# Kernel optimization log

Hardware: AMD Instinct MI355X
Metric: run time of the kernel (lower is better)

Reference implementation:

```python
import jax, jax.numpy as jnp
import numpy as np

NEG_INF = -1e9  # matches masked_fill value in torch code
LRELU_ALPHA = 0.2


def setup_inputs() -> dict:
    key = jax.random.key(0)
    k1, k2, k3, k4 = jax.random.split(key, 4)
    B, N, F_IN, H, DK = 4, 2048, 128, 4, 32
    x = jax.random.normal(k1, (B, N, F_IN), dtype=jnp.float32)
    adj = jax.random.randint(k2, (B, N, N), 0, 2, dtype=jnp.int32)
    # xavier-ish scaled params
    W = jax.random.normal(k3, (H, F_IN, DK), dtype=jnp.float32) * (1.0 / np.sqrt(F_IN))
    a = jax.random.normal(k4, (H, 2 * DK, 1), dtype=jnp.float32) * (1.0 / np.sqrt(2 * DK))
    return {"x": x, "adj": adj, "W": W, "a": a}


def reference(x, adj, W, a):
    B, N, _ = x.shape
    H, _, DK = W.shape
    # h: (B, H, N, DK)
    h = jnp.einsum('bni,hio->bhno', x, W)
    # Split attention vector: e[b,h,i,j] = h_i.a_l + h_j.a_r  (avoids O(N^2 * 2d) concat)
    a_l = a[:, :DK, 0]   # (H, DK)
    a_r = a[:, DK:, 0]   # (H, DK)
    el = jnp.einsum('bhnd,hd->bhn', h, a_l)  # (B, H, N)
    er = jnp.einsum('bhnd,hd->bhn', h, a_r)  # (B, H, N)
    e = el[:, :, :, None] + er[:, :, None, :]          # (B, H, N, N)
    e = jax.nn.leaky_relu(e, negative_slope=LRELU_ALPHA)
    e = jnp.where(adj[:, None, :, :] == 0, NEG_INF, e)
    alpha = jax.nn.softmax(e, axis=-1)                 # dropout is identity (eval)
    h_prime = jnp.einsum('bhij,bhjd->bhid', alpha, h)  # (B, H, N, DK)
    # torch code does h_prime.view(B, N, -1) on contiguous (B,H,N,DK): raw reshape
    out = h_prime.reshape(B, N, H * DK)
    return out
```

## Files before the change

### kernel.cpp

```cpp
#include <hip/hip_runtime.h>
#include <stdint.h>

#define LOG2E 1.4426950408889634f

typedef __bf16 v8bf __attribute__((ext_vector_type(8)));
typedef float v16f __attribute__((ext_vector_type(16)));

static constexpr int B = 4, N = 2048, FIN = 128, H = 4, DK = 32;
static constexpr int IT = N / 32;
static constexpr int PACK_BLOCKS = B * N * N / 1024;
static constexpr int PREP_BLOCKS = (B * N * FIN + H * DK * FIN) / 256;

__device__ __forceinline__ float exp2_fast(float x) {
#if __has_builtin(__builtin_amdgcn_exp2f)
  return __builtin_amdgcn_exp2f(x);
#else
  float r;
  asm("v_exp_f32 %0, %1" : "=v"(r) : "v"(x));
  return r;
#endif
}

__device__ __forceinline__ unsigned int bf16_rne(float f) {
  unsigned int u = __builtin_bit_cast(unsigned int, f);
  u += 0x7FFFu + ((u >> 16) & 1u);
  return u >> 16;
}

__global__ __launch_bounds__(256) void k_prep(const int* __restrict__ adj,
                                              const float* __restrict__ x,
                                              const float* __restrict__ W,
                                              unsigned int* __restrict__ adjb,
                                              unsigned short* __restrict__ xb,
                                              unsigned short* __restrict__ wtb) {
  int bid = blockIdx.x;
  int tid = threadIdx.x;
  if (bid < PACK_BLOCKS) {
    int wid = (bid * 256 + tid) >> 6;
    int lane = tid & 63;
    const int* p = adj + (size_t)wid * 256 + lane;
    unsigned long long m0 = __ballot(p[0] != 0);
    unsigned long long m1 = __ballot(p[64] != 0);
    unsigned long long m2 = __ballot(p[128] != 0);
    unsigned long long m3 = __ballot(p[192] != 0);
    if (lane == 0) {
      uint4 v0 = {(unsigned)m0, (unsigned)(m0 >> 32), (unsigned)m1, (unsigned)(m1 >> 32)};
      uint4 v1 = {(unsigned)m2, (unsigned)(m2 >> 32), (unsigned)m3, (unsigned)(m3 >> 32)};
      uint4* dst = (uint4*)(adjb + (size_t)wid * 8);
      dst[0] = v0;
      dst[1] = v1;
    }
    return;
  }
  int idx = (bid - PACK_BLOCKS) * 256 + tid;
  constexpr int TX = B * N * FIN;
  if (idx < TX) {
    xb[idx] = (unsigned short)bf16_rne(x[idx]);
  } else {
    int j = idx - TX;
    int h = j >> 12, r = j & 4095, d = r >> 7, f = r & 127;
    wtb[j] = (unsigned short)bf16_rne(W[(h * FIN + f) * DK + d]);
  }
}

__global__ __launch_bounds__(256) void k_hproj(const unsigned short* __restrict__ xb,
                                               const unsigned short* __restrict__ wtb,
                                               const float* __restrict__ a,
                                               unsigned short* __restrict__ h_t,
                                               float* __restrict__ el,
                                               float* __restrict__ er) {
  int blk = blockIdx.x;
  int b = blk >> 6, it = blk & 63;
  int tid = threadIdx.x;
  int head = tid >> 6, lane = tid & 63;
  int lrow = lane & 31, kh = lane >> 5;
  int bh = b * H + head;
  int n = it * 32 + lrow;
  const unsigned short* xp = xb + (b * N + n) * FIN + kh * 8;
  const unsigned short* wp = wtb + (head * DK + lrow) * FIN + kh * 8;
  v16f acc = {};
#pragma unroll
  for (int s = 0; s < FIN / 16; ++s) {
    v8bf av = __builtin_bit_cast(v8bf, *(const int4*)(wp + s * 16));
    v8bf bv = __builtin_bit_cast(v8bf, *(const int4*)(xp + s * 16));
    acc = __builtin_amdgcn_mfma_f32_32x32x16_bf16(av, bv, acc, 0, 0, 0);
  }
  float pel = 0.f, per = 0.f;
#pragma unroll
  for (int r = 0; r < 16; ++r) {
    int d = (r & 3) + 8 * (r >> 2) + 4 * kh;
    float hv = acc[r];
    h_t[(bh * DK + d) * N + n] = (unsigned short)bf16_rne(hv);
    pel = fmaf(hv, a[head * 2 * DK + d], pel);
    per = fmaf(hv, a[head * 2 * DK + DK + d], per);
  }
  pel += __shfl_xor(pel, 32);
  per += __shfl_xor(per, 32);
  if (kh == 0) {
    el[bh * N + n] = pel * LOG2E;
    er[bh * N + n] = per * LOG2E;
  }
}

__global__ __launch_bounds__(1024, 8) void k_attn(const unsigned int* __restrict__ adjb,
                                                  const unsigned short* __restrict__ h_t,
                                                  const float* __restrict__ el,
                                                  const float* __restrict__ er,
                                                  float* __restrict__ pnum,
                                                  float* __restrict__ pden) {
  __shared__ __align__(16) float part4[4][H][1024];
  __shared__ float lsh4[4][H][32];
  int blk = blockIdx.x;
  int bit = blk >> 1, jh = blk & 1;
  int b = bit >> 6, it = bit & 63;
  int tid = threadIdx.x;
  int wave = tid >> 6;
  int head = wave & 3, jq = wave >> 2;
  int lane = tid & 63, lrow = lane & 31, kh = lane >> 5;
  int ig = it * 32 + lrow, bh = b * H + head;

  {
    int hh = tid >> 8, jl = (tid & 255) * 4;
    *(float4*)&part4[0][hh][jl] = *(const float4*)&er[(b * H + hh) * N + jh * 1024 + jl];
  }

  float eli = el[bh * N + ig];
  int j0 = jh * 1024 + jq * 256 + kh * 8;
  const unsigned short* hp = h_t + (size_t)(bh * DK + lrow) * N + j0;
  int jql = jq * 256 + kh * 8;

  const uint4* abp = (const uint4*)(adjb + (size_t)(b * N + ig) * 64 + jh * 32 + jq * 8);
  uint4 ab0 = abp[0], ab1 = abp[1];
  unsigned adw[8] = {ab0.x, ab0.y, ab0.z, ab0.w, ab1.x, ab1.y, ab1.z, ab1.w};
  int shkh = kh * 8;

  int4 hreg0 = *(const int4*)hp;
  int4 hreg1 = *(const int4*)(hp + 16);

  __syncthreads();

  v16f acc = {};
  float lsum = 0.f;
  float4 Ea = *(const float4*)&part4[0][head][jql];
  float4 Eb = *(const float4*)&part4[0][head][jql + 4];
#pragma unroll
  for (int s = 0; s < 16; ++s) {
    int4 hb = (s & 1) ? hreg1 : hreg0;
    if (s + 2 < 16) {
      int4 nv = *(const int4*)(hp + (s + 2) * 16);
      if (s & 1) hreg1 = nv; else hreg0 = nv;
    }
    float4 ea = Ea, eb = Eb;
    if (s + 1 < 16) {
      Ea = *(const float4*)&part4[0][head][jql + (s + 1) * 16];
      Eb = *(const float4*)&part4[0][head][jql + (s + 1) * 16 + 4];
    }
    unsigned mb = (adw[s >> 1] >> (((s & 1) * 16) + shkh)) & 0xFFu;
    float ev[8] = {ea.x, ea.y, ea.z, ea.w, eb.x, eb.y, eb.z, eb.w};
    unsigned ub[8];
#pragma unroll
    for (int k = 0; k < 8; ++k) {
      float tt = eli + ev[k];
      tt = fmaxf(tt, 0.2f * tt);
      float pv = exp2_fast(tt);
      unsigned u = __builtin_bit_cast(unsigned, pv) & 0xFFFF0000u;
      u = (mb & (1u << k)) ? u : 0u;
      ub[k] = u;
      lsum += __builtin_bit_cast(float, u);
    }
    unsigned u0 = __builtin_amdgcn_perm(ub[1], ub[0], 0x07060302u);
    unsigned u1 = __builtin_amdgcn_perm(ub[3], ub[2], 0x07060302u);
    unsigned u2 = __builtin_amdgcn_perm(ub[5], ub[4], 0x07060302u);
    unsigned u3 = __builtin_amdgcn_perm(ub[7], ub[6], 0x07060302u);
    uint4 au = {u0, u1, u2, u3};
    v8bf av = __builtin_bit_cast(v8bf, au);
    v8bf hv = __builtin_bit_cast(v8bf, hb);
    acc = __builtin_amdgcn_mfma_f32_32x32x16_bf16(av, hv, acc, 0, 0, 0);
  }

  lsum += __shfl_xor(lsum, 32);
  if (lane < 32) lsh4[jq][head][lane] = lsum;

  __syncthreads();

#pragma unroll
  for (int r = 0; r < 16; ++r) {
    int rowl = (r & 3) + 8 * (r >> 2) + 4 * kh;
    part4[jq][head][rowl * 32 + lrow] = acc[r];
  }
  __syncthreads();

  int e = tid * 4;
  int rh = e >> 10, rr = e & 1023;
  float4 q0 = *(const float4*)&part4[0][rh][rr];
  float4 q1 = *(const float4*)&part4[1][rh][rr];
  float4 q2 = *(const float4*)&part4[2][rh][rr];
  float4 q3 = *(const float4*)&part4[3][rh][rr];
  float4 s4;
  s4.x = (q0.x + q1.x) + (q2.x + q3.x);
  s4.y = (q0.y + q1.y) + (q2.y + q3.y);
  s4.z = (q0.z + q1.z) + (q2.z + q3.z);
  s4.w = (q0.w + q1.w) + (q2.w + q3.w);
  *(float4*)&pnum[(size_t)blk * 4096 + e] = s4;
  if (tid < 128) {
    float d = (lsh4[0][tid >> 5][tid & 31] + lsh4[1][tid >> 5][tid & 31]) +
              (lsh4[2][tid >> 5][tid & 31] + lsh4[3][tid >> 5][tid & 31]);
    pden[blk * 128 + tid] = d;
  }
}

__global__ __launch_bounds__(1024) void k_final(const float* __restrict__ pnum,
                                                const float* __restrict__ pden,
                                                float* __restrict__ out) {
  int bit = blockIdx.x;
  int b = bit >> 6, it = bit & 63;
  int tid = threadIdx.x;
  int e = tid * 4;
  int rh = e >> 10, ri = (e >> 5) & 31, rd = e & 31;
  size_t p0 = (size_t)(bit * 2) * 4096 + e;
  float4 n0 = *(const float4*)&pnum[p0];
  float4 n1 = *(const float4*)&pnum[p0 + 4096];
  float d = pden[bit * 2 * 128 + rh * 32 + ri] + pden[(bit * 2 + 1) * 128 + rh * 32 + ri];
  float inv = 1.0f / d;
  float4 o;
  o.x = (n0.x + n1.x) * inv;
  o.y = (n0.y + n1.y) * inv;
  o.z = (n0.z + n1.z) * inv;
  o.w = (n0.w + n1.w) * inv;
  *(float4*)&out[(size_t)((b * H + rh) * N + it * 32 + ri) * DK + rd] = o;
}

extern "C" void kernel_launch(void* const* d_in, const int* in_sizes, int n_in,
                              void* d_out, int out_size, void* d_ws, size_t ws_size,
                              hipStream_t stream) {
  const float* x = (const float*)d_in[0];
  const int* adj = (const int*)d_in[1];
  const float* W = (const float*)d_in[2];
  const float* a = (const float*)d_in[3];
  float* out = (float*)d_out;
  char* ws = (char*)d_ws;

  unsigned short* h_t = (unsigned short*)(ws);
  float* el = (float*)(ws + 0x200000);
  float* er = (float*)(ws + 0x220000);
  unsigned short* wtb = (unsigned short*)(ws + 0x240000);
  unsigned int* adjb = (unsigned int*)(ws + 0x250000);
  unsigned short* xb = (unsigned short*)(ws + 0x450000);
  float* pnum = (float*)(ws + 0x650000);
  float* pden = (float*)(ws + 0xE50000);

  hipLaunchKernelGGL(k_prep, dim3(PACK_BLOCKS + PREP_BLOCKS), dim3(256), 0, stream,
                     adj, x, W, adjb, xb, wtb);
  hipLaunchKernelGGL(k_hproj, dim3(B * IT), dim3(256), 0, stream, xb, wtb, a, h_t, el, er);
  hipLaunchKernelGGL(k_attn, dim3(B * IT * 2), dim3(1024), 0, stream, adjb, h_t, el, er, pnum, pden);
  hipLaunchKernelGGL(k_final, dim3(B * IT), dim3(1024), 0, stream, pnum, pden, out);
}
```

Baseline: 128.9 us.

## Store h in MFMA fragment layout for coalesced attention B-operand loads

The projection kernel now runs a second transposed MFMA, takes the output in accumulator layout, and writes h as pre-packed per-lane bf16 MFMA fragments instead of scattered 2-byte transposed stores. The attention kernel then reads each B operand as contiguous 16-byte per-lane loads with a 512-element stride. The j indexing, adjacency mask bits and e-vector offsets are remapped to match the accumulator's interleaved k ordering. The cost is one extra MFMA chain in the projection and more intricate index bookkeeping that must match exactly.

```diff
diff --git a/kernel.cpp b/kernel.cpp
--- a/kernel.cpp
+++ b/kernel.cpp
@@ -66,7 +66,7 @@
 __global__ __launch_bounds__(256) void k_hproj(const unsigned short* __restrict__ xb,
                                                const unsigned short* __restrict__ wtb,
                                                const float* __restrict__ a,
-                                               unsigned short* __restrict__ h_t,
+                                               unsigned short* __restrict__ h_frag,
                                                float* __restrict__ el,
                                                float* __restrict__ er) {
   int blk = blockIdx.x;
@@ -79,18 +79,30 @@
   const unsigned short* xp = xb + (b * N + n) * FIN + kh * 8;
   const unsigned short* wp = wtb + (head * DK + lrow) * FIN + kh * 8;
   v16f acc = {};
+  v16f accd = {};
 #pragma unroll
   for (int s = 0; s < FIN / 16; ++s) {
     v8bf av = __builtin_bit_cast(v8bf, *(const int4*)(wp + s * 16));
     v8bf bv = __builtin_bit_cast(v8bf, *(const int4*)(xp + s * 16));
     acc = __builtin_amdgcn_mfma_f32_32x32x16_bf16(av, bv, acc, 0, 0, 0);
+    accd = __builtin_amdgcn_mfma_f32_32x32x16_bf16(bv, av, accd, 0, 0, 0);
+  }
+  {
+    unsigned w[8];
+#pragma unroll
+    for (int i = 0; i < 8; ++i)
+      w[i] = bf16_rne(accd[2 * i]) | (bf16_rne(accd[2 * i + 1]) << 16);
+    unsigned short* fp = h_frag + (((size_t)bh * 128 + it * 2) * 64 + lane) * 8;
+    int4 v0 = {(int)w[0], (int)w[1], (int)w[2], (int)w[3]};
+    int4 v1 = {(int)w[4], (int)w[5], (int)w[6], (int)w[7]};
+    *(int4*)fp = v0;
+    *(int4*)(fp + 512) = v1;
   }
   float pel = 0.f, per = 0.f;
 #pragma unroll
   for (int r = 0; r < 16; ++r) {
     int d = (r & 3) + 8 * (r >> 2) + 4 * kh;
     float hv = acc[r];
-    h_t[(bh * DK + d) * N + n] = (unsigned short)bf16_rne(hv);
     pel = fmaf(hv, a[head * 2 * DK + d], pel);
     per = fmaf(hv, a[head * 2 * DK + DK + d], per);
   }
@@ -103,7 +115,7 @@
 }
 
 __global__ __launch_bounds__(1024, 8) void k_attn(const unsigned int* __restrict__ adjb,
-                                                  const unsigned short* __restrict__ h_t,
+                                                  const unsigned short* __restrict__ h_frag,
                                                   const float* __restrict__ el,
                                                   const float* __restrict__ er,
                                                   float* __restrict__ pnum,
@@ -125,38 +137,39 @@
   }
 
   float eli = el[bh * N + ig];
-  int j0 = jh * 1024 + jq * 256 + kh * 8;
-  const unsigned short* hp = h_t + (size_t)(bh * DK + lrow) * N + j0;
-  int jql = jq * 256 + kh * 8;
+  const unsigned short* hp =
+      h_frag + (((size_t)bh * 128 + jh * 64 + jq * 16) * 64 + lane) * 8;
+  int jql = jq * 256 + 4 * kh;
 
   const uint4* abp = (const uint4*)(adjb + (size_t)(b * N + ig) * 64 + jh * 32 + jq * 8);
   uint4 ab0 = abp[0], ab1 = abp[1];
   unsigned adw[8] = {ab0.x, ab0.y, ab0.z, ab0.w, ab1.x, ab1.y, ab1.z, ab1.w};
-  int shkh = kh * 8;
+  int shkh = kh * 4;
 
   int4 hreg0 = *(const int4*)hp;
-  int4 hreg1 = *(const int4*)(hp + 16);
+  int4 hreg1 = *(const int4*)(hp + 512);
 
   __syncthreads();
 
   v16f acc = {};
   float lsum = 0.f;
   float4 Ea = *(const float4*)&part4[0][head][jql];
-  float4 Eb = *(const float4*)&part4[0][head][jql + 4];
+  float4 Eb = *(const float4*)&part4[0][head][jql + 8];
 #pragma unroll
   for (int s = 0; s < 16; ++s) {
     int4 hb = (s & 1) ? hreg1 : hreg0;
     if (s + 2 < 16) {
-      int4 nv = *(const int4*)(hp + (s + 2) * 16);
+      int4 nv = *(const int4*)(hp + (s + 2) * 512);
       if (s & 1) hreg1 = nv; else hreg0 = nv;
     }
     float4 ea = Ea, eb = Eb;
     if (s + 1 < 16) {
       Ea = *(const float4*)&part4[0][head][jql + (s + 1) * 16];
-      Eb = *(const float4*)&part4[0][head][jql + (s + 1) * 16 + 4];
-    }
-    unsigned mb = (adw[s >> 1] >> (((s & 1) * 16) + shkh)) & 0xFFu;
+      Eb = *(const float4*)&part4[0][head][jql + (s + 1) * 16 + 8];
+    }
+    unsigned mb = (adw[s >> 1] >> (((s & 1) * 16) + shkh)) & 0xF0Fu;
     float ev[8] = {ea.x, ea.y, ea.z, ea.w, eb.x, eb.y, eb.z, eb.w};
+    const unsigned mtab[8] = {1u, 2u, 4u, 8u, 0x100u, 0x200u, 0x400u, 0x800u};
     unsigned ub[8];
 #pragma unroll
     for (int k = 0; k < 8; ++k) {
@@ -164,7 +177,7 @@
       tt = fmaxf(tt, 0.2f * tt);
       float pv = exp2_fast(tt);
       unsigned u = __builtin_bit_cast(unsigned, pv) & 0xFFFF0000u;
-      u = (mb & (1u << k)) ? u : 0u;
+      u = (mb & mtab[k]) ? u : 0u;
       ub[k] = u;
       lsum += __builtin_bit_cast(float, u);
     }
@@ -240,7 +253,7 @@
   float* out = (float*)d_out;
   char* ws = (char*)d_ws;
 
-  unsigned short* h_t = (unsigned short*)(ws);
+  unsigned short* h_frag = (unsigned short*)(ws);
   float* el = (float*)(ws + 0x200000);
   float* er = (float*)(ws + 0x220000);
   unsigned short* wtb = (unsigned short*)(ws + 0x240000);
@@ -251,7 +264,7 @@
 
   hipLaunchKernelGGL(k_prep, dim3(PACK_BLOCKS + PREP_BLOCKS), dim3(256), 0, stream,
                      adj, x, W, adjb, xb, wtb);
-  hipLaunchKernelGGL(k_hproj, dim3(B * IT), dim3(256), 0, stream, xb, wtb, a, h_t, el, er);
-  hipLaunchKernelGGL(k_attn, dim3(B * IT * 2), dim3(1024), 0, stream, adjb, h_t, el, er, pnum, pden);
+  hipLaunchKernelGGL(k_hproj, dim3(B * IT), dim3(256), 0, stream, xb, wtb, a, h_frag, el, er);
+  hipLaunchKernelGGL(k_attn, dim3(B * IT * 2), dim3(1024), 0, stream, adjb, h_frag, el, er, pnum, pden);
   hipLaunchKernelGGL(k_final, dim3(B * IT), dim3(1024), 0, stream, pnum, pden, out);
 }
```

New measurement: 193.3 us. +50.0%, slower.
